# Performance work log

Hardware: AMD Instinct MI355X
Metric: run time of the kernel (lower is better)

## Reference

```python
import math
import jax, jax.numpy as jnp
import numpy as np

B, T, C, NH = 2, 2048, 2048, 16
HD = C // NH  # 128


def _quantize_int6(key, out_f, in_f):
    """Replicates Int6LinearDynamic.reset_parameters/_quantize_update."""
    w = jax.random.normal(key, (out_f, in_f), jnp.float32) * (1.0 / math.sqrt(in_f))
    max_val = jnp.clip(jnp.max(jnp.abs(w), axis=1, keepdims=True), 1e-5)
    scale = max_val / 31.0
    w_int = jnp.clip(jnp.round(w / scale), -32, 31).astype(jnp.int8)
    return w_int, scale.squeeze(1)  # [out,in] int8, [out] f32


def setup_inputs() -> dict:
    key = jax.random.key(0)
    k_x, k_a, k_p = jax.random.split(key, 3)
    attn_w, attn_scales = _quantize_int6(k_a, 3 * C, C)
    proj_w, proj_scales = _quantize_int6(k_p, C, C)
    return {
        "x": jax.random.normal(k_x, (B, T, C), jnp.float32),
        "attn_w": attn_w,
        "attn_scales": attn_scales,
        "proj_w": proj_w,
        "proj_scales": proj_scales,
        "qk_gain": jnp.float32(1.0),
    }


def _l2norm(t):
    # F.normalize(p=2, dim=-1, eps=1e-12)
    n = jnp.sqrt(jnp.sum(t * t, axis=-1, keepdims=True))
    return t / jnp.maximum(n, 1e-12)


def reference(x, attn_w, attn_scales, proj_w, proj_scales, qk_gain):
    # dequantized int6 GEMM: w = int8 * per-row scale
    wa = attn_w.astype(jnp.float32) * attn_scales[:, None]  # [3C, C]
    qkv = jnp.einsum("btc,oc->bto", x, wa)                   # [B,T,3C]
    q, k, v = jnp.split(qkv, 3, axis=2)

    def heads(t):  # [B,T,C] -> [B,NH,T,HD]
        return t.reshape(B, T, NH, HD).transpose(0, 2, 1, 3)

    q, k, v = heads(q), heads(k), heads(v)
    q = _l2norm(q) * qk_gain
    k = _l2norm(k) * qk_gain

    # causal SDPA, default scale 1/sqrt(head_dim)
    scores = jnp.einsum("bhqd,bhkd->bhqk", q, k) / math.sqrt(HD)
    causal = jnp.tril(jnp.ones((T, T), dtype=bool))
    scores = jnp.where(causal, scores, -jnp.inf)
    attn = jax.nn.softmax(scores, axis=-1)
    y = jnp.einsum("bhqk,bhkd->bhqd", attn, v)               # [B,NH,T,HD]
    y = y.transpose(0, 2, 1, 3).reshape(B, T, C)

    wp = proj_w.astype(jnp.float32) * proj_scales[:, None]   # [C, C]
    return jnp.einsum("btc,oc->bto", y, wp)
```

## Files before the change

### kernel.cpp

```cpp
#include <hip/hip_runtime.h>


#define DEVINL __device__ __forceinline__

typedef unsigned short u16;
typedef __bf16 bf16x8 __attribute__((ext_vector_type(8)));
typedef float  f32x4  __attribute__((ext_vector_type(4)));
typedef float  f32x16 __attribute__((ext_vector_type(16)));
typedef short  short8 __attribute__((ext_vector_type(8)));
typedef u16    u16x4  __attribute__((ext_vector_type(4)));
typedef unsigned uint4x __attribute__((ext_vector_type(4)));

static constexpr int T_  = 2048;
static constexpr int C_  = 2048;
static constexpr int TC3 = 6144;

DEVINL u16 f2bf(float f) {
  union { float f; unsigned u; } v; v.f = f;
  unsigned r = v.u + 0x7FFFu + ((v.u >> 16) & 1u);
  return (u16)(r >> 16);
}
DEVINL float bf2f(u16 s) {
  union { unsigned u; float f; } v; v.u = ((unsigned)s) << 16;
  return v.f;
}
DEVINL bf16x8 ld8(const u16* p) {
  return __builtin_bit_cast(bf16x8, *(const short8*)p);
}
DEVINL f32x4 mfma16(bf16x8 a, bf16x8 b, f32x4 c) {
  return __builtin_amdgcn_mfma_f32_16x16x32_bf16(a, b, c, 0, 0, 0);
}
DEVINL f32x16 mfma32(bf16x8 a, bf16x8 b, f32x16 c) {
  return __builtin_amdgcn_mfma_f32_32x32x16_bf16(a, b, c, 0, 0, 0);
}
DEVINL void async_cp16(const u16* gp, u16* lp) {
  __builtin_amdgcn_global_load_lds(
      (const __attribute__((address_space(1))) void*)gp,
      (__attribute__((address_space(3))) void*)lp, 16, 0, 0);
}
DEVINL unsigned cvtpk(float lo, float hi) {
  unsigned r;
  asm("v_cvt_pk_bf16_f32 %0, %1, %2" : "=v"(r) : "v"(lo), "v"(hi));
  return r;
}
DEVINL void plswap(unsigned& a, unsigned& b) {
  asm("v_permlane32_swap_b32 %0, %1" : "+v"(a), "+v"(b));
}
template<int N> DEVINL void vmwait() {
  if constexpr (N == 0)      asm volatile("s_waitcnt vmcnt(0)" ::: "memory");
  else if constexpr (N == 5) asm volatile("s_waitcnt vmcnt(5)" ::: "memory");
  else if constexpr (N == 7) asm volatile("s_waitcnt vmcnt(7)" ::: "memory");
  else if constexpr (N == 9) asm volatile("s_waitcnt vmcnt(9)" ::: "memory");
}

__global__ __launch_bounds__(256) void k_cast_all(
    const float* __restrict__ x, const int* __restrict__ aw,
    const int* __restrict__ pw, u16* __restrict__ xb,
    u16* __restrict__ wab, u16* __restrict__ wpb) {
  const int b = blockIdx.x;
  if (b < 8192) {
    long i = (long)(b * 256 + threadIdx.x) * 4;
    float4 v = *(const float4*)(x + i);
    u16x4 o; o.x = f2bf(v.x); o.y = f2bf(v.y); o.z = f2bf(v.z); o.w = f2bf(v.w);
    *(u16x4*)(xb + i) = o;
  } else {
    const int* in; u16* out; int lb;
    if (b < 20480) { in = aw; out = wab; lb = b - 8192; }
    else           { in = pw; out = wpb; lb = b - 20480; }
    long i = (long)(lb * 256 + threadIdx.x) * 4;
    int4 v = *(const int4*)(in + i);
    u16x4 o; o.x = f2bf((float)v.x); o.y = f2bf((float)v.y);
    o.z = f2bf((float)v.z); o.w = f2bf((float)v.w);
    *(u16x4*)(out + i) = o;
  }
}

template<int SZ>
DEVINL void stage_q(const u16* __restrict__ G, long brow, long K, int tt, int qi,
                    u16 (&L)[2][SZ], int w, int lane) {
  const int sr = w * 8 + (lane >> 3);
  const int sc = lane & 7;
  const long grow = brow + qi * 64 + sr;
  async_cp16(G + grow * K + (long)(tt << 6) + ((sc ^ (sr & 7)) << 3),
             &L[tt & 1][(qi * 64 + w * 8) * 64]);
}

template<int WP1, int WP3, bool ISS0, bool ISS123, bool LAST>
DEVINL void kstep256(int t, const u16* __restrict__ A, const u16* __restrict__ Bt,
                     long K, long bm, long bn,
                     u16 (&As)[2][256 * 64], u16 (&Bs)[2][192 * 64],
                     f32x4 (&acc)[8][3], int w, int lane) {
  const int l15 = lane & 15, quad = lane >> 4;
  const int wm = (w & 1) * 128;
  const int wn = (w >> 1) * 48;
  const int buf = t & 1;

  auto rdA = [&](int mi, int kc) -> bf16x8 {
    const int row = wm + mi * 16 + l15;
    const int k0 = kc * 32 + quad * 8;
    return ld8(&As[buf][row * 64 + (k0 ^ ((row & 7) * 8))]);
  };
  auto rdB = [&](int ni, int kc) -> bf16x8 {
    const int row = wn + ni * 16 + l15;
    const int k0 = kc * 32 + quad * 8;
    return ld8(&Bs[buf][row * 64 + (k0 ^ ((row & 7) * 8))]);
  };

  bf16x8 af[4][2], bfl[2][2];
#pragma unroll
  for (int mi = 0; mi < 4; ++mi) { af[mi][0] = rdA(mi, 0); af[mi][1] = rdA(mi, 1); }
#pragma unroll
  for (int ni = 0; ni < 2; ++ni) { bfl[ni][0] = rdB(ni, 0); bfl[ni][1] = rdB(ni, 1); }
  if constexpr (ISS0) {
    stage_q(A, bm, K, t + 1, 1, As, w, lane);
    stage_q(A, bm, K, t + 1, 3, As, w, lane);
  }
  __builtin_amdgcn_s_barrier();
  __builtin_amdgcn_s_setprio(1);
#pragma unroll
  for (int mi = 0; mi < 4; ++mi)
#pragma unroll
    for (int ni = 0; ni < 2; ++ni) {
      acc[mi][ni] = mfma16(af[mi][0], bfl[ni][0], acc[mi][ni]);
      acc[mi][ni] = mfma16(af[mi][1], bfl[ni][1], acc[mi][ni]);
    }
  __builtin_amdgcn_s_setprio(0);
  __builtin_amdgcn_s_barrier();

  bf16x8 bfh[2];
  bfh[0] = rdB(2, 0); bfh[1] = rdB(2, 1);
  if constexpr (ISS123) {
    stage_q(A, bm, K, t + 2, 0, As, w, lane);
    stage_q(A, bm, K, t + 2, 2, As, w, lane);
  }
  __builtin_amdgcn_s_barrier();
  __builtin_amdgcn_s_setprio(1);
#pragma unroll
  for (int mi = 0; mi < 4; ++mi) {
    acc[mi][2] = mfma16(af[mi][0], bfh[0], acc[mi][2]);
    acc[mi][2] = mfma16(af[mi][1], bfh[1], acc[mi][2]);
  }
  __builtin_amdgcn_s_setprio(0);
  vmwait<WP1>();
  __builtin_amdgcn_s_barrier();

  bf16x8 af2[4][2];
#pragma unroll
  for (int mi = 0; mi < 4; ++mi) { af2[mi][0] = rdA(4 + mi, 0); af2[mi][1] = rdA(4 + mi, 1); }
  if constexpr (ISS123) {
    stage_q(Bt, bn, K, t + 2, 0, Bs, w, lane);
    stage_q(Bt, bn, K, t + 2, 1, Bs, w, lane);
  }
  __builtin_amdgcn_s_barrier();
  __builtin_amdgcn_s_setprio(1);
#pragma unroll
  for (int mi = 0; mi < 4; ++mi) {
    acc[4 + mi][2] = mfma16(af2[mi][0], bfh[0], acc[4 + mi][2]);
    acc[4 + mi][2] = mfma16(af2[mi][1], bfh[1], acc[4 + mi][2]);
  }
  __builtin_amdgcn_s_setprio(0);
  __builtin_amdgcn_s_barrier();

  if constexpr (ISS123) {
    stage_q(Bt, bn, K, t + 2, 2, Bs, w, lane);
  }
  __builtin_amdgcn_s_setprio(1);
#pragma unroll
  for (int mi = 0; mi < 4; ++mi)
#pragma unroll
    for (int ni = 0; ni < 2; ++ni) {
      acc[4 + mi][ni] = mfma16(af2[mi][0], bfl[ni][0], acc[4 + mi][ni]);
      acc[4 + mi][ni] = mfma16(af2[mi][1], bfl[ni][1], acc[4 + mi][ni]);
    }
  __builtin_amdgcn_s_setprio(0);
  if constexpr (!LAST) {
    vmwait<WP3>();
    __builtin_amdgcn_s_barrier();
  }
}

__global__ __launch_bounds__(512, 2) void k_gemm256(
    const u16* __restrict__ A, const u16* __restrict__ Bt,
    const float* __restrict__ scale, u16* __restrict__ C,
    int N, long K) {
  __shared__ u16 As[2][256 * 64];
  __shared__ u16 Bs[2][192 * 64];
  const int tid = threadIdx.x, w = tid >> 6, lane = tid & 63;
  const long bm = (long)blockIdx.y * 256;
  const long bn = (long)blockIdx.x * 192;
  const int nt = (int)(K >> 6);

  stage_q(A, bm, K, 0, 0, As, w, lane); stage_q(A, bm, K, 0, 2, As, w, lane);
  stage_q(Bt, bn, K, 0, 0, Bs, w, lane); stage_q(Bt, bn, K, 0, 1, Bs, w, lane);
  stage_q(Bt, bn, K, 0, 2, Bs, w, lane);
  stage_q(A, bm, K, 0, 1, As, w, lane); stage_q(A, bm, K, 0, 3, As, w, lane);
  stage_q(A, bm, K, 1, 0, As, w, lane); stage_q(A, bm, K, 1, 2, As, w, lane);
  stage_q(Bt, bn, K, 1, 0, Bs, w, lane); stage_q(Bt, bn, K, 1, 1, Bs, w, lane);
  stage_q(Bt, bn, K, 1, 2, Bs, w, lane);
  vmwait<5>();
  __builtin_amdgcn_s_barrier();

  f32x4 acc[8][3] = {};
  int t = 0;
  for (; t < nt - 2; ++t)
    kstep256<9, 5, true, true, false>(t, A, Bt, K, bm, bn, As, Bs, acc, w, lane);
  kstep256<7, 0, true, false, false>(nt - 2, A, Bt, K, bm, bn, As, Bs, acc, w, lane);
  kstep256<0, 0, false, false, true>(nt - 1, A, Bt, K, bm, bn, As, Bs, acc, w, lane);

  const int l15 = lane & 15, quad = lane >> 4;
  const int wm = (w & 1) * 128, wn = (w >> 1) * 48;
#pragma unroll
  for (int ni = 0; ni < 3; ++ni) {
    const long col = bn + wn + ni * 16 + l15;
    const float sc = scale[col];
#pragma unroll
    for (int mi = 0; mi < 8; ++mi) {
      const long row0 = bm + wm + mi * 16 + quad * 4;
#pragma unroll
      for (int r = 0; r < 4; ++r)
        C[(row0 + r) * (long)N + col] = f2bf(acc[mi][ni][r] * sc);
    }
  }
}

__global__ __launch_bounds__(512, 2) void k_gemm_proj(
    const u16* __restrict__ A, const u16* __restrict__ Bt,
    const float* __restrict__ scale, float* __restrict__ C,
    int N, long K) {
  __shared__ u16 As[2][128 * 64];
  __shared__ u16 Bs[2][256 * 64];
  const int tid = threadIdx.x, w = tid >> 6, lane = tid & 63;
  const int l15 = lane & 15, quad = lane >> 4;
  const int wm = (w & 1) * 64, wn = (w >> 1) * 64;
  const long bm = (long)blockIdx.y * 128;
  const long bn = (long)blockIdx.x * 256;
  const int nt = (int)(K >> 6);

  auto rdA = [&](int mi, int kc, int buf) -> bf16x8 {
    const int row = wm + mi * 16 + l15;
    const int k0 = kc * 32 + quad * 8;
    return ld8(&As[buf][row * 64 + (k0 ^ ((row & 7) * 8))]);
  };
  auto rdB = [&](int ni, int kc, int buf) -> bf16x8 {
    const int row = wn + ni * 16 + l15;
    const int k0 = kc * 32 + quad * 8;
    return ld8(&Bs[buf][row * 64 + (k0 ^ ((row & 7) * 8))]);
  };

  stage_q(A, bm, K, 0, 0, As, w, lane); stage_q(A, bm, K, 0, 1, As, w, lane);
  stage_q(Bt, bn, K, 0, 0, Bs, w, lane); stage_q(Bt, bn, K, 0, 1, Bs, w, lane);
  stage_q(Bt, bn, K, 0, 2, Bs, w, lane); stage_q(Bt, bn, K, 0, 3, Bs, w, lane);
  vmwait<0>();
  __builtin_amdgcn_s_barrier();

  f32x4 acc[4][4] = {};
  for (int t = 0; t < nt; ++t) {
    const int buf = t & 1;
    const bool iss = (t < nt - 1);
    bf16x8 a01[2][2], a23[2][2], b01[2][2], b23[2][2];

    if (iss) {
      stage_q(Bt, bn, K, t + 1, 0, Bs, w, lane);
      stage_q(Bt, bn, K, t + 1, 1, Bs, w, lane);
      stage_q(A,  bm, K, t + 1, 0, As, w, lane);
    }
#pragma unroll
    for (int mi = 0; mi < 2; ++mi) { a01[mi][0] = rdA(mi, 0, buf); a01[mi][1] = rdA(mi, 1, buf); }
#pragma unroll
    for (int ni = 0; ni < 2; ++ni) { b01[ni][0] = rdB(ni, 0, buf); b01[ni][1] = rdB(ni, 1, buf); }
    __builtin_amdgcn_s_barrier();
    __builtin_amdgcn_s_setprio(1);
#pragma unroll
    for (int mi = 0; mi < 2; ++mi)
#pragma unroll
      for (int ni = 0; ni < 2; ++ni) {
        acc[mi][ni] = mfma16(a01[mi][0], b01[ni][0], acc[mi][ni]);
        acc[mi][ni] = mfma16(a01[mi][1], b01[ni][1], acc[mi][ni]);
      }
    __builtin_amdgcn_s_setprio(0);
    __builtin_amdgcn_s_barrier();

    if (iss) {
      stage_q(Bt, bn, K, t + 1, 2, Bs, w, lane);
      stage_q(Bt, bn, K, t + 1, 3, Bs, w, lane);
      stage_q(A,  bm, K, t + 1, 1, As, w, lane);
    }
#pragma unroll
    for (int ni = 0; ni < 2; ++ni) { b23[ni][0] = rdB(2 + ni, 0, buf); b23[ni][1] = rdB(2 + ni, 1, buf); }
    __builtin_amdgcn_s_barrier();
    __builtin_amdgcn_s_setprio(1);
#pragma unroll
    for (int mi = 0; mi < 2; ++mi)
#pragma unroll
      for (int ni = 0; ni < 2; ++ni) {
        acc[mi][2 + ni] = mfma16(a01[mi][0], b23[ni][0], acc[mi][2 + ni]);
        acc[mi][2 + ni] = mfma16(a01[mi][1], b23[ni][1], acc[mi][2 + ni]);
      }
    __builtin_amdgcn_s_setprio(0);
    __builtin_amdgcn_s_barrier();

#pragma unroll
    for (int mi = 0; mi < 2; ++mi) { a23[mi][0] = rdA(2 + mi, 0, buf); a23[mi][1] = rdA(2 + mi, 1, buf); }
    __builtin_amdgcn_s_barrier();
    __builtin_amdgcn_s_setprio(1);
#pragma unroll
    for (int mi = 0; mi < 2; ++mi)
#pragma unroll
      for (int ni = 0; ni < 2; ++ni) {
        acc[2 + mi][2 + ni] = mfma16(a23[mi][0], b23[ni][0], acc[2 + mi][2 + ni]);
        acc[2 + mi][2 + ni] = mfma16(a23[mi][1], b23[ni][1], acc[2 + mi][2 + ni]);
      }
    __builtin_amdgcn_s_setprio(0);
    __builtin_amdgcn_s_barrier();

    __builtin_amdgcn_s_setprio(1);
#pragma unroll
    for (int mi = 0; mi < 2; ++mi)
#pragma unroll
      for (int ni = 0; ni < 2; ++ni) {
        acc[2 + mi][ni] = mfma16(a23[mi][0], b01[ni][0], acc[2 + mi][ni]);
        acc[2 + mi][ni] = mfma16(a23[mi][1], b01[ni][1], acc[2 + mi][ni]);
      }
    __builtin_amdgcn_s_setprio(0);
    if (iss) {
      vmwait<0>();
      __builtin_amdgcn_s_barrier();
    }
  }

#pragma unroll
  for (int ni = 0; ni < 4; ++ni) {
    const long col = bn + wn + ni * 16 + l15;
    const float sc = scale[col];
#pragma unroll
    for (int mi = 0; mi < 4; ++mi) {
      const long row0 = bm + wm + mi * 16 + quad * 4;
#pragma unroll
      for (int r = 0; r < 4; ++r)
        C[(row0 + r) * (long)N + col] = acc[mi][ni][r] * sc;
    }
  }
}

__global__ __launch_bounds__(256) void k_norm_vt(u16* __restrict__ qkv,
                                                 const float* __restrict__ qk_gain,
                                                 u16* __restrict__ vt) {
  const int b = blockIdx.x;
  if (b < 4096) {
    const int token = b;
    const int wave = threadIdx.x >> 6, lane = threadIdx.x & 63;
    const float g = qk_gain[0];
    const float qmul = g * g * 1.44269504f * 0.08838834764f;
    u16* rowp = qkv + (long)token * TC3;
#pragma unroll
    for (int s = 0; s < 8; ++s) {
      const int seg = wave * 8 + s;
      const int isK = seg >> 4;
      const int h = seg & 15;
      u16* ptr = rowp + isK * C_ + h * 128 + lane * 2;
      unsigned pv = *(const unsigned*)ptr;
      float a = bf2f((u16)(pv & 0xffffu));
      float bb = bf2f((u16)(pv >> 16));
      float ss = a * a + bb * bb;
#pragma unroll
      for (int m = 1; m <= 32; m <<= 1) ss += __shfl_xor(ss, m);
      float denom = fmaxf(sqrtf(ss), 1e-12f);
      float f = (isK ? 1.0f : qmul) / denom;
      u16 o0 = f2bf(a * f), o1 = f2bf(bb * f);
      *(unsigned*)ptr = (unsigned)o0 | ((unsigned)o1 << 16);
    }
  } else {
    const int v = b - 4096;
    const int t0 = (v & 31) * 64;
    const int h = (v >> 5) & 15;
    const int bz = v >> 9;
    const int t = threadIdx.x & 63;
    const int d0 = threadIdx.x >> 6;
    const long tokbase = (long)bz * T_;
    const u16* src = qkv + (tokbase + t0 + t) * (long)TC3 + 2 * C_ + h * 128;
    u16* dst = vt + ((long)(bz * 16 + h) * 128) * (long)T_ + t0 + t;
#pragma unroll
    for (int dd = 0; dd < 32; ++dd) {
      const int d = dd * 4 + d0;
      dst[(long)d * T_] = src[d];
    }
  }
}

__global__ __launch_bounds__(256, 2) void k_attn(const u16* __restrict__ qkv,
                                                 const u16* __restrict__ vtg,
                                                 u16* __restrict__ y) {
  const int qt = blockIdx.z ? (15 - blockIdx.x) : blockIdx.x;
  const int h  = blockIdx.y;
  const int bz = blockIdx.z;
  const int tid = threadIdx.x, w = tid >> 6, lane = tid & 63;
  const int m31 = lane & 31, hi = lane >> 5;

  __shared__ u16 Ks[2][64 * 128];
  __shared__ u16 Vt[2][128 * 64];

  const long tokbase = (long)bz * T_;
  const int qbase = qt * 128 + w * 32;
  const u16* vbase = vtg + ((long)(bz * 16 + h) * 128) * (long)T_;
  const u16* kbase = qkv + tokbase * TC3 + C_ + h * 128;

  bf16x8 qf[8];
  {
    const u16* qp = qkv + (tokbase + qbase + m31) * (long)TC3 + h * 128 + hi * 8;
#pragma unroll
    for (int kc = 0; kc < 8; ++kc)
      qf[kc] = ld8(qp + kc * 16);
  }

  f32x16 o[4];
#pragma unroll
  for (int i = 0; i < 4; ++i)
#pragma unroll
    for (int r = 0; r < 16; ++r) o[i][r] = 0.f;
  f32x4 lacc = {0.f, 0.f, 0.f, 0.f};

  auto stage = [&](int ktb, int b2) {
#pragma unroll
    for (int j = 0; j < 4; ++j) {
      const int t = w * 4 + j;
      const int p = t * 64 + lane;
      const int r  = p >> 4, ck = p & 15;
      async_cp16(kbase + (long)(ktb + r) * TC3 + ((ck ^ (r & 15)) * 8),
                 &Ks[b2][t * 512]);
      const int d  = p >> 3, cv = p & 7;
      async_cp16(vbase + (long)d * T_ + ktb + ((cv ^ (d & 7)) * 8),
                 &Vt[b2][t * 512]);
    }
  };

  stage(0, 0);
  __syncthreads();
  int b = 0;
  const int ktmax = 2 * qt + 1;

  for (int kt = 0; kt <= ktmax; ++kt) {
    const int ktb = kt * 64;
    if (kt < ktmax) stage(ktb + 64, b ^ 1);

    if (ktb <= qbase + 31) {
      f32x16 sA[2];
      __builtin_amdgcn_s_setprio(1);
#pragma unroll
      for (int kb = 0; kb < 2; ++kb) {
        f32x16 acc;
#pragma unroll
        for (int r = 0; r < 16; ++r) acc[r] = 0.f;
#pragma unroll
        for (int kc = 0; kc < 8; ++kc) {
          bf16x8 kf = ld8(&Ks[b][(kb * 32 + m31) * 128 +
                                 (((2 * kc + hi) ^ (lane & 15)) * 8)]);
          acc = mfma32(kf, qf[kc], acc);
        }
        sA[kb] = acc;
      }
      __builtin_amdgcn_s_setprio(0);

      if (ktb + 63 > qbase) {
        const int qq = qbase + m31;
#pragma unroll
        for (int kb = 0; kb < 2; ++kb)
#pragma unroll
          for (int r = 0; r < 16; ++r) {
            const int key = ktb + kb * 32 + (r & 3) + 8 * (r >> 2) + 4 * hi;
            if (key > qq) sA[kb][r] = -1e30f;
          }
      }
#pragma unroll
      for (int kb = 0; kb < 2; ++kb)
#pragma unroll
        for (int r = 0; r < 16; ++r) {
          float p = __builtin_amdgcn_exp2f(sA[kb][r]);
          sA[kb][r] = p;
          lacc[r & 3] += p;
        }

      bf16x8 pb[4];
#pragma unroll
      for (int ks = 0; ks < 4; ++ks) {
        const int kb = ks >> 1, j = ks & 1;
        unsigned w0a = cvtpk(sA[kb][8 * j + 0], sA[kb][8 * j + 1]);
        unsigned w1a = cvtpk(sA[kb][8 * j + 2], sA[kb][8 * j + 3]);
        unsigned w0b = cvtpk(sA[kb][8 * j + 4], sA[kb][8 * j + 5]);
        unsigned w1b = cvtpk(sA[kb][8 * j + 6], sA[kb][8 * j + 7]);
        plswap(w0a, w0b);
        plswap(w1a, w1b);
        uint4x t; t.x = w0a; t.y = w1a; t.z = w0b; t.w = w1b;
        pb[ks] = __builtin_bit_cast(bf16x8, t);
      }

      __builtin_amdgcn_s_setprio(1);
#pragma unroll
      for (int db = 0; db < 4; ++db)
#pragma unroll
        for (int ks = 0; ks < 4; ++ks) {
          bf16x8 vf = ld8(&Vt[b][(db * 32 + m31) * 64 +
                                 (((2 * ks + hi) ^ (m31 & 7)) * 8)]);
          o[db] = mfma32(vf, pb[ks], o[db]);
        }
      __builtin_amdgcn_s_setprio(0);
    }

    if (kt < ktmax) __syncthreads();
    b ^= 1;
  }

  float lrow = lacc[0] + lacc[1] + lacc[2] + lacc[3];
  lrow += __shfl_xor(lrow, 32);
  const float inv_l = 1.0f / lrow;
  u16* yp = y + (tokbase + qbase + m31) * (long)C_ + h * 128 + 4 * hi;
#pragma unroll
  for (int db = 0; db < 4; ++db)
#pragma unroll
    for (int g = 0; g < 4; ++g) {
      u16x4 pk;
#pragma unroll
      for (int r = 0; r < 4; ++r) pk[r] = f2bf(o[db][g * 4 + r] * inv_l);
      *(u16x4*)(yp + db * 32 + g * 8) = pk;
    }
}

extern "C" void kernel_launch(void* const* d_in, const int* in_sizes, int n_in,
                              void* d_out, int out_size, void* d_ws, size_t ws_size,
                              hipStream_t stream) {
  const float* x    = (const float*)d_in[0];
  const int*   aw   = (const int*)d_in[1];
  const float* asc  = (const float*)d_in[2];
  const int*   pw   = (const int*)d_in[3];
  const float* psc  = (const float*)d_in[4];
  const float* gain = (const float*)d_in[5];

  char* ws = (char*)d_ws;
  u16* xb  = (u16*)(ws);
  u16* wab = (u16*)(ws + 16777216UL);
  u16* wpb = (u16*)(ws + 41943040UL);
  u16* qkv = (u16*)(ws + 50331648UL);
  u16* yb  = (u16*)(ws + 100663296UL);
  u16* vtg = xb;

  k_cast_all<<<24576, 256, 0, stream>>>(x, aw, pw, xb, wab, wpb);
  k_gemm256<<<dim3(32, 16), 512, 0, stream>>>(xb, wab, asc, qkv, TC3, (long)C_);
  k_norm_vt<<<5120, 256, 0, stream>>>(qkv, gain, vtg);
  k_attn<<<dim3(16, 16, 2), 256, 0, stream>>>(qkv, vtg, yb);
  k_gemm_proj<<<dim3(8, 32), 512, 0, stream>>>(yb, wpb, psc, (float*)d_out, C_, (long)C_);
}
```

Measured before the change: 416.3 us.

## Rewrite QKV GEMM with 256x384 tiles, K-step 32, and a chunked LDS layout

The QKV projection GEMM moves from 256x192 tiles with a 64-wide K step and an XOR-swizzled LDS layout to 256x384 tiles with a 32-wide K step. LDS now holds contiguous 8-row by 32-column chunks, and the grid shrinks to 16x16 blocks. The larger N tile is meant to raise operand reuse per LDS load and cut global traffic, and the simpler loop drops the hand-tuned partial vmcnt waits. In exchange, each step now ends with a full vmcnt(0) wait, the prefetch runs only one step ahead, and 256 blocks may underfill the GPU while the 48 accumulators per lane raise register pressure.

```diff
diff --git a/kernel.cpp b/kernel.cpp
--- a/kernel.cpp
+++ b/kernel.cpp
@@ -48,9 +48,6 @@
 }
 template<int N> DEVINL void vmwait() {
   if constexpr (N == 0)      asm volatile("s_waitcnt vmcnt(0)" ::: "memory");
-  else if constexpr (N == 5) asm volatile("s_waitcnt vmcnt(5)" ::: "memory");
-  else if constexpr (N == 7) asm volatile("s_waitcnt vmcnt(7)" ::: "memory");
-  else if constexpr (N == 9) asm volatile("s_waitcnt vmcnt(9)" ::: "memory");
 }
 
 __global__ __launch_bounds__(256) void k_cast_all(
@@ -76,6 +73,100 @@
 }
 
 template<int SZ>
+DEVINL void stage32(const u16* __restrict__ G, long brow, long K, int tt, int qi,
+                    u16 (&L)[2][SZ], int w, int lane) {
+  const int p  = w * 64 + lane;
+  const int r8 = p & 7;
+  const int ck = (p >> 3) & 3;
+  const int q  = p >> 5;
+  const long row = brow + qi * 128 + q * 8 + r8;
+  async_cp16(G + row * K + (long)(tt << 5) + ck * 8,
+             &L[tt & 1][(qi * 512 + w * 64) * 8]);
+}
+
+__global__ __launch_bounds__(512, 2) void k_gemm256(
+    const u16* __restrict__ A, const u16* __restrict__ Bt,
+    const float* __restrict__ scale, u16* __restrict__ C,
+    int N, long K) {
+  __shared__ u16 As[2][256 * 32];
+  __shared__ u16 Bs[2][384 * 32];
+  const int tid = threadIdx.x, w = tid >> 6, lane = tid & 63;
+  const int l15 = lane & 15, quad = lane >> 4;
+  const int wm = (w & 1) * 128;
+  const int wn = (w >> 1) * 96;
+  const long bm = (long)blockIdx.y * 256;
+  const long bn = (long)blockIdx.x * 384;
+  const int nt = (int)(K >> 5);
+
+  const int abase = ((wm >> 3) + (l15 >> 3)) * 32 + quad * 8 + (l15 & 7);
+  const int bbase = ((wn >> 3) + (l15 >> 3)) * 32 + quad * 8 + (l15 & 7);
+
+  stage32(A,  bm, K, 0, 0, As, w, lane); stage32(A,  bm, K, 0, 1, As, w, lane);
+  stage32(Bt, bn, K, 0, 0, Bs, w, lane); stage32(Bt, bn, K, 0, 1, Bs, w, lane);
+  stage32(Bt, bn, K, 0, 2, Bs, w, lane);
+  vmwait<0>();
+  __builtin_amdgcn_s_barrier();
+
+  f32x4 acc[8][6] = {};
+  for (int t = 0; t < nt; ++t) {
+    const int buf = t & 1;
+    const bool iss = (t < nt - 1);
+    bf16x8 bfr[6], afr[4];
+
+    if (iss) {
+      stage32(A,  bm, K, t + 1, 0, As, w, lane);
+      stage32(A,  bm, K, t + 1, 1, As, w, lane);
+      stage32(Bt, bn, K, t + 1, 0, Bs, w, lane);
+    }
+#pragma unroll
+    for (int ni = 0; ni < 6; ++ni) bfr[ni] = ld8(&Bs[buf][(bbase + ni * 64) * 8]);
+#pragma unroll
+    for (int mi = 0; mi < 4; ++mi) afr[mi] = ld8(&As[buf][(abase + mi * 64) * 8]);
+    __builtin_amdgcn_s_barrier();
+    __builtin_amdgcn_s_setprio(1);
+#pragma unroll
+    for (int mi = 0; mi < 4; ++mi)
+#pragma unroll
+      for (int ni = 0; ni < 6; ++ni)
+        acc[mi][ni] = mfma16(afr[mi], bfr[ni], acc[mi][ni]);
+    __builtin_amdgcn_s_setprio(0);
+    __builtin_amdgcn_s_barrier();
+
+    if (iss) {
+      stage32(Bt, bn, K, t + 1, 1, Bs, w, lane);
+      stage32(Bt, bn, K, t + 1, 2, Bs, w, lane);
+    }
+#pragma unroll
+    for (int mi = 0; mi < 4; ++mi) afr[mi] = ld8(&As[buf][(abase + (4 + mi) * 64) * 8]);
+    __builtin_amdgcn_s_barrier();
+    __builtin_amdgcn_s_setprio(1);
+#pragma unroll
+    for (int mi = 0; mi < 4; ++mi)
+#pragma unroll
+      for (int ni = 0; ni < 6; ++ni)
+        acc[4 + mi][ni] = mfma16(afr[mi], bfr[ni], acc[4 + mi][ni]);
+    __builtin_amdgcn_s_setprio(0);
+    if (iss) {
+      vmwait<0>();
+      __builtin_amdgcn_s_barrier();
+    }
+  }
+
+#pragma unroll
+  for (int ni = 0; ni < 6; ++ni) {
+    const long col = bn + wn + ni * 16 + l15;
+    const float sc = scale[col];
+#pragma unroll
+    for (int mi = 0; mi < 8; ++mi) {
+      const long row0 = bm + wm + mi * 16 + quad * 4;
+#pragma unroll
+      for (int r = 0; r < 4; ++r)
+        C[(row0 + r) * (long)N + col] = f2bf(acc[mi][ni][r] * sc);
+    }
+  }
+}
+
+template<int SZ>
 DEVINL void stage_q(const u16* __restrict__ G, long brow, long K, int tt, int qi,
                     u16 (&L)[2][SZ], int w, int lane) {
   const int sr = w * 8 + (lane >> 3);
@@ -83,144 +174,6 @@
   const long grow = brow + qi * 64 + sr;
   async_cp16(G + grow * K + (long)(tt << 6) + ((sc ^ (sr & 7)) << 3),
              &L[tt & 1][(qi * 64 + w * 8) * 64]);
-}
-
-template<int WP1, int WP3, bool ISS0, bool ISS123, bool LAST>
-DEVINL void kstep256(int t, const u16* __restrict__ A, const u16* __restrict__ Bt,
-                     long K, long bm, long bn,
-                     u16 (&As)[2][256 * 64], u16 (&Bs)[2][192 * 64],
-                     f32x4 (&acc)[8][3], int w, int lane) {
-  const int l15 = lane & 15, quad = lane >> 4;
-  const int wm = (w & 1) * 128;
-  const int wn = (w >> 1) * 48;
-  const int buf = t & 1;
-
-  auto rdA = [&](int mi, int kc) -> bf16x8 {
-    const int row = wm + mi * 16 + l15;
-    const int k0 = kc * 32 + quad * 8;
-    return ld8(&As[buf][row * 64 + (k0 ^ ((row & 7) * 8))]);
-  };
-  auto rdB = [&](int ni, int kc) -> bf16x8 {
-    const int row = wn + ni * 16 + l15;
-    const int k0 = kc * 32 + quad * 8;
-    return ld8(&Bs[buf][row * 64 + (k0 ^ ((row & 7) * 8))]);
-  };
-
-  bf16x8 af[4][2], bfl[2][2];
-#pragma unroll
-  for (int mi = 0; mi < 4; ++mi) { af[mi][0] = rdA(mi, 0); af[mi][1] = rdA(mi, 1); }
-#pragma unroll
-  for (int ni = 0; ni < 2; ++ni) { bfl[ni][0] = rdB(ni, 0); bfl[ni][1] = rdB(ni, 1); }
-  if constexpr (ISS0) {
-    stage_q(A, bm, K, t + 1, 1, As, w, lane);
-    stage_q(A, bm, K, t + 1, 3, As, w, lane);
-  }
-  __builtin_amdgcn_s_barrier();
-  __builtin_amdgcn_s_setprio(1);
-#pragma unroll
-  for (int mi = 0; mi < 4; ++mi)
-#pragma unroll
-    for (int ni = 0; ni < 2; ++ni) {
-      acc[mi][ni] = mfma16(af[mi][0], bfl[ni][0], acc[mi][ni]);
-      acc[mi][ni] = mfma16(af[mi][1], bfl[ni][1], acc[mi][ni]);
-    }
-  __builtin_amdgcn_s_setprio(0);
-  __builtin_amdgcn_s_barrier();
-
-  bf16x8 bfh[2];
-  bfh[0] = rdB(2, 0); bfh[1] = rdB(2, 1);
-  if constexpr (ISS123) {
-    stage_q(A, bm, K, t + 2, 0, As, w, lane);
-    stage_q(A, bm, K, t + 2, 2, As, w, lane);
-  }
-  __builtin_amdgcn_s_barrier();
-  __builtin_amdgcn_s_setprio(1);
-#pragma unroll
-  for (int mi = 0; mi < 4; ++mi) {
-    acc[mi][2] = mfma16(af[mi][0], bfh[0], acc[mi][2]);
-    acc[mi][2] = mfma16(af[mi][1], bfh[1], acc[mi][2]);
-  }
-  __builtin_amdgcn_s_setprio(0);
-  vmwait<WP1>();
-  __builtin_amdgcn_s_barrier();
-
-  bf16x8 af2[4][2];
-#pragma unroll
-  for (int mi = 0; mi < 4; ++mi) { af2[mi][0] = rdA(4 + mi, 0); af2[mi][1] = rdA(4 + mi, 1); }
-  if constexpr (ISS123) {
-    stage_q(Bt, bn, K, t + 2, 0, Bs, w, lane);
-    stage_q(Bt, bn, K, t + 2, 1, Bs, w, lane);
-  }
-  __builtin_amdgcn_s_barrier();
-  __builtin_amdgcn_s_setprio(1);
-#pragma unroll
-  for (int mi = 0; mi < 4; ++mi) {
-    acc[4 + mi][2] = mfma16(af2[mi][0], bfh[0], acc[4 + mi][2]);
-    acc[4 + mi][2] = mfma16(af2[mi][1], bfh[1], acc[4 + mi][2]);
-  }
-  __builtin_amdgcn_s_setprio(0);
-  __builtin_amdgcn_s_barrier();
-
-  if constexpr (ISS123) {
-    stage_q(Bt, bn, K, t + 2, 2, Bs, w, lane);
-  }
-  __builtin_amdgcn_s_setprio(1);
-#pragma unroll
-  for (int mi = 0; mi < 4; ++mi)
-#pragma unroll
-    for (int ni = 0; ni < 2; ++ni) {
-      acc[4 + mi][ni] = mfma16(af2[mi][0], bfl[ni][0], acc[4 + mi][ni]);
-      acc[4 + mi][ni] = mfma16(af2[mi][1], bfl[ni][1], acc[4 + mi][ni]);
-    }
-  __builtin_amdgcn_s_setprio(0);
-  if constexpr (!LAST) {
-    vmwait<WP3>();
-    __builtin_amdgcn_s_barrier();
-  }
-}
-
-__global__ __launch_bounds__(512, 2) void k_gemm256(
-    const u16* __restrict__ A, const u16* __restrict__ Bt,
-    const float* __restrict__ scale, u16* __restrict__ C,
-    int N, long K) {
-  __shared__ u16 As[2][256 * 64];
-  __shared__ u16 Bs[2][192 * 64];
-  const int tid = threadIdx.x, w = tid >> 6, lane = tid & 63;
-  const long bm = (long)blockIdx.y * 256;
-  const long bn = (long)blockIdx.x * 192;
-  const int nt = (int)(K >> 6);
-
-  stage_q(A, bm, K, 0, 0, As, w, lane); stage_q(A, bm, K, 0, 2, As, w, lane);
-  stage_q(Bt, bn, K, 0, 0, Bs, w, lane); stage_q(Bt, bn, K, 0, 1, Bs, w, lane);
-  stage_q(Bt, bn, K, 0, 2, Bs, w, lane);
-  stage_q(A, bm, K, 0, 1, As, w, lane); stage_q(A, bm, K, 0, 3, As, w, lane);
-  stage_q(A, bm, K, 1, 0, As, w, lane); stage_q(A, bm, K, 1, 2, As, w, lane);
-  stage_q(Bt, bn, K, 1, 0, Bs, w, lane); stage_q(Bt, bn, K, 1, 1, Bs, w, lane);
-  stage_q(Bt, bn, K, 1, 2, Bs, w, lane);
-  vmwait<5>();
-  __builtin_amdgcn_s_barrier();
-
-  f32x4 acc[8][3] = {};
-  int t = 0;
-  for (; t < nt - 2; ++t)
-    kstep256<9, 5, true, true, false>(t, A, Bt, K, bm, bn, As, Bs, acc, w, lane);
-  kstep256<7, 0, true, false, false>(nt - 2, A, Bt, K, bm, bn, As, Bs, acc, w, lane);
-  kstep256<0, 0, false, false, true>(nt - 1, A, Bt, K, bm, bn, As, Bs, acc, w, lane);
-
-  const int l15 = lane & 15, quad = lane >> 4;
-  const int wm = (w & 1) * 128, wn = (w >> 1) * 48;
-#pragma unroll
-  for (int ni = 0; ni < 3; ++ni) {
-    const long col = bn + wn + ni * 16 + l15;
-    const float sc = scale[col];
-#pragma unroll
-    for (int mi = 0; mi < 8; ++mi) {
-      const long row0 = bm + wm + mi * 16 + quad * 4;
-#pragma unroll
-      for (int r = 0; r < 4; ++r)
-        C[(row0 + r) * (long)N + col] = f2bf(acc[mi][ni][r] * sc);
-    }
-  }
 }
 
 __global__ __launch_bounds__(512, 2) void k_gemm_proj(
@@ -543,7 +496,7 @@
   u16* vtg = xb;
 
   k_cast_all<<<24576, 256, 0, stream>>>(x, aw, pw, xb, wab, wpb);
-  k_gemm256<<<dim3(32, 16), 512, 0, stream>>>(xb, wab, asc, qkv, TC3, (long)C_);
+  k_gemm256<<<dim3(16, 16), 512, 0, stream>>>(xb, wab, asc, qkv, TC3, (long)C_);
   k_norm_vt<<<5120, 256, 0, stream>>>(qkv, gain, vtg);
   k_attn<<<dim3(16, 16, 2), 256, 0, stream>>>(qkv, vtg, yb);
   k_gemm_proj<<<dim3(8, 32), 512, 0, stream>>>(yb, wpb, psc, (float*)d_out, C_, (long)C_);
```

After: 455.4 us. +9.4%, slower.

## Split attention key tiles across two wave teams with shared-memory reduction

Applied to the files above, without the earlier changes.

Doubles the attention block to 512 threads. Two teams of four waves each handle half of every 64-key tile for the same 32-query slices, so each wave does half the QK and PV MFMAs per tile, and async staging work is spread across more waves. At the end, team 1 writes its partial output accumulators and row sums through LDS, reusing the K/V buffers, and team 0 adds them before normalising and storing. This raises per-block parallelism and latency hiding, at the cost of an extra reduction pass, two extra barriers, and possibly lower occupancy from register and LDS pressure with the larger block.

```diff
diff --git a/kernel.cpp b/kernel.cpp
--- a/kernel.cpp
+++ b/kernel.cpp
@@ -387,7 +387,7 @@
   }
 }
 
-__global__ __launch_bounds__(256, 2) void k_attn(const u16* __restrict__ qkv,
+__global__ __launch_bounds__(512, 4) void k_attn(const u16* __restrict__ qkv,
                                                  const u16* __restrict__ vtg,
                                                  u16* __restrict__ y) {
   const int qt = blockIdx.z ? (15 - blockIdx.x) : blockIdx.x;
@@ -395,12 +395,14 @@
   const int bz = blockIdx.z;
   const int tid = threadIdx.x, w = tid >> 6, lane = tid & 63;
   const int m31 = lane & 31, hi = lane >> 5;
+  const int team = w >> 2, ws = w & 3;
 
   __shared__ u16 Ks[2][64 * 128];
   __shared__ u16 Vt[2][128 * 64];
+  __shared__ float lr[4][64];
 
   const long tokbase = (long)bz * T_;
-  const int qbase = qt * 128 + w * 32;
+  const int qbase = qt * 128 + ws * 32;
   const u16* vbase = vtg + ((long)(bz * 16 + h) * 128) * (long)T_;
   const u16* kbase = qkv + tokbase * TC3 + C_ + h * 128;
 
@@ -421,8 +423,8 @@
 
   auto stage = [&](int ktb, int b2) {
 #pragma unroll
-    for (int j = 0; j < 4; ++j) {
-      const int t = w * 4 + j;
+    for (int j = 0; j < 2; ++j) {
+      const int t = w * 2 + j;
       const int p = t * 64 + lane;
       const int r  = p >> 4, ck = p & 15;
       async_cp16(kbase + (long)(ktb + r) * TC3 + ((ck ^ (r & 15)) * 8),
@@ -442,65 +444,57 @@
     const int ktb = kt * 64;
     if (kt < ktmax) stage(ktb + 64, b ^ 1);
 
-    if (ktb <= qbase + 31) {
-      f32x16 sA[2];
+    const int kteam = ktb + team * 32;
+    if (kteam <= qbase + 31) {
+      f32x16 sA;
+#pragma unroll
+      for (int r = 0; r < 16; ++r) sA[r] = 0.f;
       __builtin_amdgcn_s_setprio(1);
 #pragma unroll
-      for (int kb = 0; kb < 2; ++kb) {
-        f32x16 acc;
-#pragma unroll
-        for (int r = 0; r < 16; ++r) acc[r] = 0.f;
-#pragma unroll
-        for (int kc = 0; kc < 8; ++kc) {
-          bf16x8 kf = ld8(&Ks[b][(kb * 32 + m31) * 128 +
-                                 (((2 * kc + hi) ^ (lane & 15)) * 8)]);
-          acc = mfma32(kf, qf[kc], acc);
+      for (int kc = 0; kc < 8; ++kc) {
+        bf16x8 kf = ld8(&Ks[b][(team * 32 + m31) * 128 +
+                               (((2 * kc + hi) ^ (lane & 15)) * 8)]);
+        sA = mfma32(kf, qf[kc], sA);
+      }
+      __builtin_amdgcn_s_setprio(0);
+
+      if (kteam + 31 > qbase) {
+        const int qq = qbase + m31;
+#pragma unroll
+        for (int r = 0; r < 16; ++r) {
+          const int key = kteam + (r & 3) + 8 * (r >> 2) + 4 * hi;
+          if (key > qq) sA[r] = -1e30f;
         }
-        sA[kb] = acc;
-      }
-      __builtin_amdgcn_s_setprio(0);
-
-      if (ktb + 63 > qbase) {
-        const int qq = qbase + m31;
-#pragma unroll
-        for (int kb = 0; kb < 2; ++kb)
-#pragma unroll
-          for (int r = 0; r < 16; ++r) {
-            const int key = ktb + kb * 32 + (r & 3) + 8 * (r >> 2) + 4 * hi;
-            if (key > qq) sA[kb][r] = -1e30f;
-          }
-      }
-#pragma unroll
-      for (int kb = 0; kb < 2; ++kb)
-#pragma unroll
-        for (int r = 0; r < 16; ++r) {
-          float p = __builtin_amdgcn_exp2f(sA[kb][r]);
-          sA[kb][r] = p;
-          lacc[r & 3] += p;
-        }
-
-      bf16x8 pb[4];
-#pragma unroll
-      for (int ks = 0; ks < 4; ++ks) {
-        const int kb = ks >> 1, j = ks & 1;
-        unsigned w0a = cvtpk(sA[kb][8 * j + 0], sA[kb][8 * j + 1]);
-        unsigned w1a = cvtpk(sA[kb][8 * j + 2], sA[kb][8 * j + 3]);
-        unsigned w0b = cvtpk(sA[kb][8 * j + 4], sA[kb][8 * j + 5]);
-        unsigned w1b = cvtpk(sA[kb][8 * j + 6], sA[kb][8 * j + 7]);
+      }
+#pragma unroll
+      for (int r = 0; r < 16; ++r) {
+        float p = __builtin_amdgcn_exp2f(sA[r]);
+        sA[r] = p;
+        lacc[r & 3] += p;
+      }
+
+      bf16x8 pb[2];
+#pragma unroll
+      for (int j = 0; j < 2; ++j) {
+        unsigned w0a = cvtpk(sA[8 * j + 0], sA[8 * j + 1]);
+        unsigned w1a = cvtpk(sA[8 * j + 2], sA[8 * j + 3]);
+        unsigned w0b = cvtpk(sA[8 * j + 4], sA[8 * j + 5]);
+        unsigned w1b = cvtpk(sA[8 * j + 6], sA[8 * j + 7]);
         plswap(w0a, w0b);
         plswap(w1a, w1b);
         uint4x t; t.x = w0a; t.y = w1a; t.z = w0b; t.w = w1b;
-        pb[ks] = __builtin_bit_cast(bf16x8, t);
+        pb[j] = __builtin_bit_cast(bf16x8, t);
       }
 
       __builtin_amdgcn_s_setprio(1);
 #pragma unroll
       for (int db = 0; db < 4; ++db)
 #pragma unroll
-        for (int ks = 0; ks < 4; ++ks) {
+        for (int kl = 0; kl < 2; ++kl) {
+          const int ks = team * 2 + kl;
           bf16x8 vf = ld8(&Vt[b][(db * 32 + m31) * 64 +
                                  (((2 * ks + hi) ^ (m31 & 7)) * 8)]);
-          o[db] = mfma32(vf, pb[ks], o[db]);
+          o[db] = mfma32(vf, pb[kl], o[db]);
         }
       __builtin_amdgcn_s_setprio(0);
     }
@@ -511,17 +505,43 @@
 
   float lrow = lacc[0] + lacc[1] + lacc[2] + lacc[3];
   lrow += __shfl_xor(lrow, 32);
-  const float inv_l = 1.0f / lrow;
-  u16* yp = y + (tokbase + qbase + m31) * (long)C_ + h * 128 + 4 * hi;
-#pragma unroll
-  for (int db = 0; db < 4; ++db)
-#pragma unroll
-    for (int g = 0; g < 4; ++g) {
-      u16x4 pk;
-#pragma unroll
-      for (int r = 0; r < 4; ++r) pk[r] = f2bf(o[db][g * 4 + r] * inv_l);
-      *(u16x4*)(yp + db * 32 + g * 8) = pk;
-    }
+
+  __syncthreads();
+  {
+    float* ex = (ws == 0) ? (float*)&Ks[0][0]
+              : (ws == 1) ? (float*)&Ks[1][0]
+              : (ws == 2) ? (float*)&Vt[0][0]
+              :             (float*)&Vt[1][0];
+    if (team == 1) {
+#pragma unroll
+      for (int db = 0; db < 4; ++db)
+#pragma unroll
+        for (int r = 0; r < 16; ++r)
+          ex[(db * 16 + r) * 64 + lane] = o[db][r];
+      lr[ws][lane] = lrow;
+    }
+    __syncthreads();
+    if (team == 0) {
+#pragma unroll
+      for (int db = 0; db < 4; ++db)
+#pragma unroll
+        for (int r = 0; r < 16; ++r)
+          o[db][r] += ex[(db * 16 + r) * 64 + lane];
+      lrow += lr[ws][lane];
+
+      const float inv_l = 1.0f / lrow;
+      u16* yp = y + (tokbase + qbase + m31) * (long)C_ + h * 128 + 4 * hi;
+#pragma unroll
+      for (int db = 0; db < 4; ++db)
+#pragma unroll
+        for (int g = 0; g < 4; ++g) {
+          u16x4 pk;
+#pragma unroll
+          for (int r = 0; r < 4; ++r) pk[r] = f2bf(o[db][g * 4 + r] * inv_l);
+          *(u16x4*)(yp + db * 32 + g * 8) = pk;
+        }
+    }
+  }
 }
 
 extern "C" void kernel_launch(void* const* d_in, const int* in_sizes, int n_in,
@@ -545,6 +565,6 @@
   k_cast_all<<<24576, 256, 0, stream>>>(x, aw, pw, xb, wab, wpb);
   k_gemm256<<<dim3(32, 16), 512, 0, stream>>>(xb, wab, asc, qkv, TC3, (long)C_);
   k_norm_vt<<<5120, 256, 0, stream>>>(qkv, gain, vtg);
-  k_attn<<<dim3(16, 16, 2), 256, 0, stream>>>(qkv, vtg, yb);
+  k_attn<<<dim3(16, 16, 2), 512, 0, stream>>>(qkv, vtg, yb);
   k_gemm_proj<<<dim3(8, 32), 512, 0, stream>>>(yb, wpb, psc, (float*)d_out, C_, (long)C_);
 }
```

After: 470.4 us. 13.0% more time.

## Prefetch two K-tiles ahead in projection GEMM with partial vmcnt waits

Applied to the files above, without the earlier changes.

The projection GEMM now issues global-to-LDS loads for tile t+2 instead of t+1. Each step waits only on the older batch of loads (vmcnt(6)) rather than draining all outstanding loads, so memory latency overlaps more compute. The loop body moves into a templated step function with peeled final iterations. The loads for t+2 go into the same double buffer, issued after the reads of the current buffer. This relies on barrier placement to avoid overwriting data still being read, which is a correctness risk.

```diff
diff --git a/kernel.cpp b/kernel.cpp
--- a/kernel.cpp
+++ b/kernel.cpp
@@ -49,6 +49,7 @@
 template<int N> DEVINL void vmwait() {
   if constexpr (N == 0)      asm volatile("s_waitcnt vmcnt(0)" ::: "memory");
   else if constexpr (N == 5) asm volatile("s_waitcnt vmcnt(5)" ::: "memory");
+  else if constexpr (N == 6) asm volatile("s_waitcnt vmcnt(6)" ::: "memory");
   else if constexpr (N == 7) asm volatile("s_waitcnt vmcnt(7)" ::: "memory");
   else if constexpr (N == 9) asm volatile("s_waitcnt vmcnt(9)" ::: "memory");
 }
@@ -223,6 +224,97 @@
   }
 }
 
+template<bool ISS, bool LAST, int WEND>
+DEVINL void pstep(int t, const u16* __restrict__ A, const u16* __restrict__ Bt,
+                  long K, long bm, long bn,
+                  u16 (&As)[2][128 * 64], u16 (&Bs)[2][256 * 64],
+                  f32x4 (&acc)[4][4], int w, int lane) {
+  const int l15 = lane & 15, quad = lane >> 4;
+  const int wm = (w & 1) * 64, wn = (w >> 1) * 64;
+  const int buf = t & 1;
+
+  auto rdA = [&](int mi, int kc) -> bf16x8 {
+    const int row = wm + mi * 16 + l15;
+    const int k0 = kc * 32 + quad * 8;
+    return ld8(&As[buf][row * 64 + (k0 ^ ((row & 7) * 8))]);
+  };
+  auto rdB = [&](int ni, int kc) -> bf16x8 {
+    const int row = wn + ni * 16 + l15;
+    const int k0 = kc * 32 + quad * 8;
+    return ld8(&Bs[buf][row * 64 + (k0 ^ ((row & 7) * 8))]);
+  };
+
+  bf16x8 a01[2][2], a23[2][2], b01[2][2], b23[2][2];
+
+#pragma unroll
+  for (int mi = 0; mi < 2; ++mi) { a01[mi][0] = rdA(mi, 0); a01[mi][1] = rdA(mi, 1); }
+#pragma unroll
+  for (int ni = 0; ni < 2; ++ni) { b01[ni][0] = rdB(ni, 0); b01[ni][1] = rdB(ni, 1); }
+  __builtin_amdgcn_s_barrier();
+  __builtin_amdgcn_s_setprio(1);
+#pragma unroll
+  for (int mi = 0; mi < 2; ++mi)
+#pragma unroll
+    for (int ni = 0; ni < 2; ++ni) {
+      acc[mi][ni] = mfma16(a01[mi][0], b01[ni][0], acc[mi][ni]);
+      acc[mi][ni] = mfma16(a01[mi][1], b01[ni][1], acc[mi][ni]);
+    }
+  __builtin_amdgcn_s_setprio(0);
+  __builtin_amdgcn_s_barrier();
+
+#pragma unroll
+  for (int ni = 0; ni < 2; ++ni) { b23[ni][0] = rdB(2 + ni, 0); b23[ni][1] = rdB(2 + ni, 1); }
+  __builtin_amdgcn_s_barrier();
+  __builtin_amdgcn_s_setprio(1);
+#pragma unroll
+  for (int mi = 0; mi < 2; ++mi)
+#pragma unroll
+    for (int ni = 0; ni < 2; ++ni) {
+      acc[mi][2 + ni] = mfma16(a01[mi][0], b23[ni][0], acc[mi][2 + ni]);
+      acc[mi][2 + ni] = mfma16(a01[mi][1], b23[ni][1], acc[mi][2 + ni]);
+    }
+  __builtin_amdgcn_s_setprio(0);
+  __builtin_amdgcn_s_barrier();
+
+  if constexpr (ISS) {
+    stage_q(Bt, bn, K, t + 2, 0, Bs, w, lane);
+    stage_q(Bt, bn, K, t + 2, 1, Bs, w, lane);
+    stage_q(Bt, bn, K, t + 2, 2, Bs, w, lane);
+    stage_q(Bt, bn, K, t + 2, 3, Bs, w, lane);
+  }
+#pragma unroll
+  for (int mi = 0; mi < 2; ++mi) { a23[mi][0] = rdA(2 + mi, 0); a23[mi][1] = rdA(2 + mi, 1); }
+  __builtin_amdgcn_s_barrier();
+  __builtin_amdgcn_s_setprio(1);
+#pragma unroll
+  for (int mi = 0; mi < 2; ++mi)
+#pragma unroll
+    for (int ni = 0; ni < 2; ++ni) {
+      acc[2 + mi][2 + ni] = mfma16(a23[mi][0], b23[ni][0], acc[2 + mi][2 + ni]);
+      acc[2 + mi][2 + ni] = mfma16(a23[mi][1], b23[ni][1], acc[2 + mi][2 + ni]);
+    }
+  __builtin_amdgcn_s_setprio(0);
+  __builtin_amdgcn_s_barrier();
+
+  if constexpr (ISS) {
+    stage_q(A, bm, K, t + 2, 0, As, w, lane);
+    stage_q(A, bm, K, t + 2, 1, As, w, lane);
+  }
+  __builtin_amdgcn_s_setprio(1);
+#pragma unroll
+  for (int mi = 0; mi < 2; ++mi)
+#pragma unroll
+    for (int ni = 0; ni < 2; ++ni) {
+      acc[2 + mi][ni] = mfma16(a23[mi][0], b01[ni][0], acc[2 + mi][ni]);
+      acc[2 + mi][ni] = mfma16(a23[mi][1], b01[ni][1], acc[2 + mi][ni]);
+    }
+  __builtin_amdgcn_s_setprio(0);
+  if constexpr (!LAST) {
+    vmwait<WEND>();
+    __builtin_amdgcn_s_barrier();
+  }
+}
+
 __global__ __launch_bounds__(512, 2) void k_gemm_proj(
     const u16* __restrict__ A, const u16* __restrict__ Bt,
     const float* __restrict__ scale, float* __restrict__ C,
@@ -230,104 +322,28 @@
   __shared__ u16 As[2][128 * 64];
   __shared__ u16 Bs[2][256 * 64];
   const int tid = threadIdx.x, w = tid >> 6, lane = tid & 63;
-  const int l15 = lane & 15, quad = lane >> 4;
-  const int wm = (w & 1) * 64, wn = (w >> 1) * 64;
   const long bm = (long)blockIdx.y * 128;
   const long bn = (long)blockIdx.x * 256;
   const int nt = (int)(K >> 6);
 
-  auto rdA = [&](int mi, int kc, int buf) -> bf16x8 {
-    const int row = wm + mi * 16 + l15;
-    const int k0 = kc * 32 + quad * 8;
-    return ld8(&As[buf][row * 64 + (k0 ^ ((row & 7) * 8))]);
-  };
-  auto rdB = [&](int ni, int kc, int buf) -> bf16x8 {
-    const int row = wn + ni * 16 + l15;
-    const int k0 = kc * 32 + quad * 8;
-    return ld8(&Bs[buf][row * 64 + (k0 ^ ((row & 7) * 8))]);
-  };
-
   stage_q(A, bm, K, 0, 0, As, w, lane); stage_q(A, bm, K, 0, 1, As, w, lane);
   stage_q(Bt, bn, K, 0, 0, Bs, w, lane); stage_q(Bt, bn, K, 0, 1, Bs, w, lane);
   stage_q(Bt, bn, K, 0, 2, Bs, w, lane); stage_q(Bt, bn, K, 0, 3, Bs, w, lane);
-  vmwait<0>();
+  stage_q(A, bm, K, 1, 0, As, w, lane); stage_q(A, bm, K, 1, 1, As, w, lane);
+  stage_q(Bt, bn, K, 1, 0, Bs, w, lane); stage_q(Bt, bn, K, 1, 1, Bs, w, lane);
+  stage_q(Bt, bn, K, 1, 2, Bs, w, lane); stage_q(Bt, bn, K, 1, 3, Bs, w, lane);
+  vmwait<6>();
   __builtin_amdgcn_s_barrier();
 
   f32x4 acc[4][4] = {};
-  for (int t = 0; t < nt; ++t) {
-    const int buf = t & 1;
-    const bool iss = (t < nt - 1);
-    bf16x8 a01[2][2], a23[2][2], b01[2][2], b23[2][2];
-
-    if (iss) {
-      stage_q(Bt, bn, K, t + 1, 0, Bs, w, lane);
-      stage_q(Bt, bn, K, t + 1, 1, Bs, w, lane);
-      stage_q(A,  bm, K, t + 1, 0, As, w, lane);
-    }
-#pragma unroll
-    for (int mi = 0; mi < 2; ++mi) { a01[mi][0] = rdA(mi, 0, buf); a01[mi][1] = rdA(mi, 1, buf); }
-#pragma unroll
-    for (int ni = 0; ni < 2; ++ni) { b01[ni][0] = rdB(ni, 0, buf); b01[ni][1] = rdB(ni, 1, buf); }
-    __builtin_amdgcn_s_barrier();
-    __builtin_amdgcn_s_setprio(1);
-#pragma unroll
-    for (int mi = 0; mi < 2; ++mi)
-#pragma unroll
-      for (int ni = 0; ni < 2; ++ni) {
-        acc[mi][ni] = mfma16(a01[mi][0], b01[ni][0], acc[mi][ni]);
-        acc[mi][ni] = mfma16(a01[mi][1], b01[ni][1], acc[mi][ni]);
-      }
-    __builtin_amdgcn_s_setprio(0);
-    __builtin_amdgcn_s_barrier();
-
-    if (iss) {
-      stage_q(Bt, bn, K, t + 1, 2, Bs, w, lane);
-      stage_q(Bt, bn, K, t + 1, 3, Bs, w, lane);
-      stage_q(A,  bm, K, t + 1, 1, As, w, lane);
-    }
-#pragma unroll
-    for (int ni = 0; ni < 2; ++ni) { b23[ni][0] = rdB(2 + ni, 0, buf); b23[ni][1] = rdB(2 + ni, 1, buf); }
-    __builtin_amdgcn_s_barrier();
-    __builtin_amdgcn_s_setprio(1);
-#pragma unroll
-    for (int mi = 0; mi < 2; ++mi)
-#pragma unroll
-      for (int ni = 0; ni < 2; ++ni) {
-        acc[mi][2 + ni] = mfma16(a01[mi][0], b23[ni][0], acc[mi][2 + ni]);
-        acc[mi][2 + ni] = mfma16(a01[mi][1], b23[ni][1], acc[mi][2 + ni]);
-      }
-    __builtin_amdgcn_s_setprio(0);
-    __builtin_amdgcn_s_barrier();
-
-#pragma unroll
-    for (int mi = 0; mi < 2; ++mi) { a23[mi][0] = rdA(2 + mi, 0, buf); a23[mi][1] = rdA(2 + mi, 1, buf); }
-    __builtin_amdgcn_s_barrier();
-    __builtin_amdgcn_s_setprio(1);
-#pragma unroll
-    for (int mi = 0; mi < 2; ++mi)
-#pragma unroll
-      for (int ni = 0; ni < 2; ++ni) {
-        acc[2 + mi][2 + ni] = mfma16(a23[mi][0], b23[ni][0], acc[2 + mi][2 + ni]);
-        acc[2 + mi][2 + ni] = mfma16(a23[mi][1], b23[ni][1], acc[2 + mi][2 + ni]);
-      }
-    __builtin_amdgcn_s_setprio(0);
-    __builtin_amdgcn_s_barrier();
-
-    __builtin_amdgcn_s_setprio(1);
-#pragma unroll
-    for (int mi = 0; mi < 2; ++mi)
-#pragma unroll
-      for (int ni = 0; ni < 2; ++ni) {
-        acc[2 + mi][ni] = mfma16(a23[mi][0], b01[ni][0], acc[2 + mi][ni]);
-        acc[2 + mi][ni] = mfma16(a23[mi][1], b01[ni][1], acc[2 + mi][ni]);
-      }
-    __builtin_amdgcn_s_setprio(0);
-    if (iss) {
-      vmwait<0>();
-      __builtin_amdgcn_s_barrier();
-    }
-  }
-
+  int t = 0;
+  for (; t < nt - 2; ++t)
+    pstep<true, false, 6>(t, A, Bt, K, bm, bn, As, Bs, acc, w, lane);
+  pstep<false, false, 0>(nt - 2, A, Bt, K, bm, bn, As, Bs, acc, w, lane);
+  pstep<false, true, 0>(nt - 1, A, Bt, K, bm, bn, As, Bs, acc, w, lane);
+
+  const int l15 = lane & 15, quad = lane >> 4;
+  const int wm = (w & 1) * 64, wn = (w >> 1) * 64;
 #pragma unroll
   for (int ni = 0; ni < 4; ++ni) {
     const long col = bn + wn + ni * 16 + l15;
```

Result: faster. 396.9 us (-4.7%).
